# Kernel tuning notes

Hardware: AMD Instinct MI355X
Metric: run time of the kernel (lower is better)

## Reference

```python
import jax, jax.numpy as jnp
import numpy as np

CAPACITY = 0.75      # MoDRouter capacity
ACT_STEPS = 3        # act_max_steps
EPS = 0.01           # ACT halting epsilon
PONDER = 0.01        # act_ponder_cost


def setup_inputs() -> dict:
    key = jax.random.key(0)
    k1, k2, k3 = jax.random.split(key, 3)
    x = jax.random.normal(k1, (4, 8192, 1024), dtype=jnp.float32)
    router_w = jax.random.normal(k2, (1024,), dtype=jnp.float32) * 0.02  # nn.Linear(dim,1,bias=False), std=0.02
    halt_w = jax.random.normal(k3, (1024,), dtype=jnp.float32) * 0.02    # halt linear weight (zeros-init in src; perturbed for nontrivial signal)
    halt_b = -jnp.ones((1,), dtype=jnp.float32)                          # halt bias init -1.0
    return {"x": x, "router_w": router_w, "halt_w": halt_w, "halt_b": halt_b}


def _mod_step(x, router_w):
    """MoDRouter.forward + identity block + MoDRouter.scatter_back."""
    b, s, d = x.shape
    k = max(1, int(s * CAPACITY))
    scores = jnp.einsum('bsd,d->bs', x, router_w)                 # (b, s)
    topk_scores, idx = jax.lax.top_k(scores, k)                   # sorted desc, like torch.topk
    routed = jnp.take_along_axis(x, idx[:, :, None], axis=1)      # (b, k, d) gather
    processed = routed                                            # identity stand-in for Block (undefined in source)
    w = jax.nn.softmax(topk_scores, axis=1)[:, :, None]           # straight-through weights (b, k, 1)
    new_vals = processed * w + (1.0 - w) * routed                 # weighted_processed + (1-w)*original_at_indices
    return x.at[jnp.arange(b)[:, None], idx].set(new_vals)        # scatter back; unrouted tokens = identity


def _act_combine(states, halt_w, halt_b):
    """ACTHaltingUnit.forward: masked accumulation over recurrence steps."""
    b, s, d = states[0].shape
    dt = states[0].dtype
    acc = jnp.zeros((b, s), dt)
    out = jnp.zeros((b, s, d), dt)
    rem = jnp.ones((b, s), dt)
    n_upd = jnp.zeros((b, s), dt)
    for state in states:  # fixed small loop over recurrence steps
        h = jax.nn.sigmoid(jnp.einsum('bsd,d->bs', state, halt_w) + halt_b[0])
        still = (acc < 1.0 - EPS).astype(dt)
        new_acc = acc + h * still
        use_rem = (new_acc > 1.0 - EPS).astype(dt) * still
        use_h = (1.0 - use_rem) * still
        p = use_h * h + use_rem * rem
        out = out + p[:, :, None] * state
        acc = acc + p * still
        rem = rem - p * still
        n_upd = n_upd + still
    ponder_loss = PONDER * jnp.mean(n_upd)
    return out, ponder_loss


def reference(x, router_w, halt_w, halt_b):
    states = []
    cur = x
    for _ in range(ACT_STEPS):
        cur = _mod_step(cur, router_w)
        states.append(cur)
    return _act_combine(states, halt_w, halt_b)
```

## Files before the change

### kernel.cpp

```cpp
#include <hip/hip_runtime.h>
#include <math.h>

#define N_TOKENS 32768
#define DIM      1024
#define WAVES_PER_BLOCK 4

__global__ void modgpt_init(int* __restrict__ n_acc) {
    if (threadIdx.x == 0 && blockIdx.x == 0) n_acc[0] = 0;
}

__global__ __launch_bounds__(256) void modgpt_main(
        const float* __restrict__ x,
        const float* __restrict__ halt_w,
        const float* __restrict__ halt_b,
        float* __restrict__ out,
        int* __restrict__ n_acc) {
    const int wave = threadIdx.x >> 6;
    const int lane = threadIdx.x & 63;
    const int token = blockIdx.x * WAVES_PER_BLOCK + wave;

    const float4* __restrict__ xin = (const float4*)(x + (size_t)token * DIM);
    const float4* __restrict__ w4  = (const float4*)halt_w;

    float4 v0 = xin[lane];
    float4 v1 = xin[lane + 64];
    float4 v2 = xin[lane + 128];
    float4 v3 = xin[lane + 192];
    float4 w0 = w4[lane];
    float4 w1 = w4[lane + 64];
    float4 w2 = w4[lane + 128];
    float4 w3 = w4[lane + 192];

    float dot = v0.x * w0.x + v0.y * w0.y + v0.z * w0.z + v0.w * w0.w
              + v1.x * w1.x + v1.y * w1.y + v1.z * w1.z + v1.w * w1.w
              + v2.x * w2.x + v2.y * w2.y + v2.z * w2.z + v2.w * w2.w
              + v3.x * w3.x + v3.y * w3.y + v3.z * w3.z + v3.w * w3.w;

    #pragma unroll
    for (int off = 32; off >= 1; off >>= 1)
        dot += __shfl_xor(dot, off, 64);

    const float h = 1.0f / (1.0f + expf(-(dot + halt_b[0])));

    float acc = 0.0f, rem = 1.0f, P = 0.0f;
    int n = 0;
    #pragma unroll
    for (int s = 0; s < 3; ++s) {
        if (acc < 0.99f) {
            const float na = acc + h;
            const float p  = (na > 0.99f) ? rem : h;
            P   += p;
            acc += p;
            rem -= p;
            n   += 1;
        }
    }

    float4* __restrict__ o = (float4*)(out + (size_t)token * DIM);
    v0.x *= P; v0.y *= P; v0.z *= P; v0.w *= P;
    v1.x *= P; v1.y *= P; v1.z *= P; v1.w *= P;
    v2.x *= P; v2.y *= P; v2.z *= P; v2.w *= P;
    v3.x *= P; v3.y *= P; v3.z *= P; v3.w *= P;
    o[lane]       = v0;
    o[lane + 64]  = v1;
    o[lane + 128] = v2;
    o[lane + 192] = v3;

    __shared__ int sn[WAVES_PER_BLOCK];
    if (lane == 0) sn[wave] = n;
    __syncthreads();
    if (threadIdx.x == 0)
        atomicAdd(n_acc, sn[0] + sn[1] + sn[2] + sn[3]);
}

__global__ void modgpt_finalize(const int* __restrict__ n_acc,
                                float* __restrict__ ponder_out) {
    if (threadIdx.x == 0 && blockIdx.x == 0)
        ponder_out[0] = 0.01f * ((float)n_acc[0] / (float)N_TOKENS);
}

extern "C" void kernel_launch(void* const* d_in, const int* in_sizes, int n_in,
                              void* d_out, int out_size, void* d_ws, size_t ws_size,
                              hipStream_t stream) {
    const float* x        = (const float*)d_in[0];
    const float* halt_w   = (const float*)d_in[2];
    const float* halt_b   = (const float*)d_in[3];
    float* out            = (float*)d_out;
    int*   n_acc          = (int*)d_ws;

    modgpt_init<<<1, 64, 0, stream>>>(n_acc);
    modgpt_main<<<N_TOKENS / WAVES_PER_BLOCK, 256, 0, stream>>>(
        x, halt_w, halt_b, out, n_acc);
    modgpt_finalize<<<1, 64, 0, stream>>>(n_acc, out + (size_t)N_TOKENS * DIM);
}
```

Before: 272.5 us.

## Process eight tokens per wave with register prefetch and nontemporal stores

Each wave now handles eight consecutive tokens instead of one. It software-pipelines by loading the next token's row while reducing and scaling the current one. The halting weights and bias are loaded once per wave, and the output uses nontemporal stores to avoid polluting cache, with one eighth as many blocks and atomics. The trade-offs are a grid 8x smaller, with fewer waves in flight to hide memory latency, and higher register pressure from the double-buffered rows.

```diff
diff --git a/kernel.cpp b/kernel.cpp
--- a/kernel.cpp
+++ b/kernel.cpp
@@ -4,6 +4,9 @@
 #define N_TOKENS 32768
 #define DIM      1024
 #define WAVES_PER_BLOCK 4
+#define TOK_PER_WAVE 8
+
+typedef float v4f __attribute__((ext_vector_type(4)));
 
 __global__ void modgpt_init(int* __restrict__ n_acc) {
     if (threadIdx.x == 0 && blockIdx.x == 0) n_acc[0] = 0;
@@ -17,57 +20,70 @@
         int* __restrict__ n_acc) {
     const int wave = threadIdx.x >> 6;
     const int lane = threadIdx.x & 63;
-    const int token = blockIdx.x * WAVES_PER_BLOCK + wave;
+    const int token0 = (blockIdx.x * WAVES_PER_BLOCK + wave) * TOK_PER_WAVE;
 
-    const float4* __restrict__ xin = (const float4*)(x + (size_t)token * DIM);
-    const float4* __restrict__ w4  = (const float4*)halt_w;
+    const v4f* __restrict__ xin = (const v4f*)(x + (size_t)token0 * DIM);
+    v4f* __restrict__ oout      = (v4f*)(out + (size_t)token0 * DIM);
+    const v4f* __restrict__ w4  = (const v4f*)halt_w;
 
-    float4 v0 = xin[lane];
-    float4 v1 = xin[lane + 64];
-    float4 v2 = xin[lane + 128];
-    float4 v3 = xin[lane + 192];
-    float4 w0 = w4[lane];
-    float4 w1 = w4[lane + 64];
-    float4 w2 = w4[lane + 128];
-    float4 w3 = w4[lane + 192];
+    const v4f w0 = w4[lane];
+    const v4f w1 = w4[lane + 64];
+    const v4f w2 = w4[lane + 128];
+    const v4f w3 = w4[lane + 192];
+    const float hb = halt_b[0];
 
-    float dot = v0.x * w0.x + v0.y * w0.y + v0.z * w0.z + v0.w * w0.w
-              + v1.x * w1.x + v1.y * w1.y + v1.z * w1.z + v1.w * w1.w
-              + v2.x * w2.x + v2.y * w2.y + v2.z * w2.z + v2.w * w2.w
-              + v3.x * w3.x + v3.y * w3.y + v3.z * w3.z + v3.w * w3.w;
+    int n_sum = 0;
+
+    v4f c0 = xin[lane];
+    v4f c1 = xin[lane + 64];
+    v4f c2 = xin[lane + 128];
+    v4f c3 = xin[lane + 192];
 
     #pragma unroll
-    for (int off = 32; off >= 1; off >>= 1)
-        dot += __shfl_xor(dot, off, 64);
+    for (int t = 0; t < TOK_PER_WAVE; ++t) {
+        v4f p0, p1, p2, p3;
+        if (t + 1 < TOK_PER_WAVE) {
+            const v4f* nx = xin + (size_t)(t + 1) * 256;
+            p0 = nx[lane];
+            p1 = nx[lane + 64];
+            p2 = nx[lane + 128];
+            p3 = nx[lane + 192];
+        }
 
-    const float h = 1.0f / (1.0f + expf(-(dot + halt_b[0])));
+        v4f m = c0 * w0 + c1 * w1 + c2 * w2 + c3 * w3;
+        float dot = m.x + m.y + m.z + m.w;
+        #pragma unroll
+        for (int off = 32; off >= 1; off >>= 1)
+            dot += __shfl_xor(dot, off, 64);
 
-    float acc = 0.0f, rem = 1.0f, P = 0.0f;
-    int n = 0;
-    #pragma unroll
-    for (int s = 0; s < 3; ++s) {
-        if (acc < 0.99f) {
-            const float na = acc + h;
-            const float p  = (na > 0.99f) ? rem : h;
-            P   += p;
-            acc += p;
-            rem -= p;
-            n   += 1;
+        const float h = 1.0f / (1.0f + expf(-(dot + hb)));
+
+        float acc = 0.0f, rem = 1.0f, P = 0.0f;
+        int n = 0;
+        #pragma unroll
+        for (int s = 0; s < 3; ++s) {
+            if (acc < 0.99f) {
+                const float na = acc + h;
+                const float p  = (na > 0.99f) ? rem : h;
+                P   += p;
+                acc += p;
+                rem -= p;
+                n   += 1;
+            }
         }
+        n_sum += n;
+
+        v4f* op = oout + (size_t)t * 256;
+        __builtin_nontemporal_store(c0 * P, op + lane);
+        __builtin_nontemporal_store(c1 * P, op + lane + 64);
+        __builtin_nontemporal_store(c2 * P, op + lane + 128);
+        __builtin_nontemporal_store(c3 * P, op + lane + 192);
+
+        c0 = p0; c1 = p1; c2 = p2; c3 = p3;
     }
 
-    float4* __restrict__ o = (float4*)(out + (size_t)token * DIM);
-    v0.x *= P; v0.y *= P; v0.z *= P; v0.w *= P;
-    v1.x *= P; v1.y *= P; v1.z *= P; v1.w *= P;
-    v2.x *= P; v2.y *= P; v2.z *= P; v2.w *= P;
-    v3.x *= P; v3.y *= P; v3.z *= P; v3.w *= P;
-    o[lane]       = v0;
-    o[lane + 64]  = v1;
-    o[lane + 128] = v2;
-    o[lane + 192] = v3;
-
     __shared__ int sn[WAVES_PER_BLOCK];
-    if (lane == 0) sn[wave] = n;
+    if (lane == 0) sn[wave] = n_sum;
     __syncthreads();
     if (threadIdx.x == 0)
         atomicAdd(n_acc, sn[0] + sn[1] + sn[2] + sn[3]);
@@ -89,7 +105,7 @@
     int*   n_acc          = (int*)d_ws;
 
     modgpt_init<<<1, 64, 0, stream>>>(n_acc);
-    modgpt_main<<<N_TOKENS / WAVES_PER_BLOCK, 256, 0, stream>>>(
+    modgpt_main<<<N_TOKENS / (WAVES_PER_BLOCK * TOK_PER_WAVE), 256, 0, stream>>>(
         x, halt_w, halt_b, out, n_acc);
     modgpt_finalize<<<1, 64, 0, stream>>>(n_acc, out + (size_t)N_TOKENS * DIM);
 }
```

After: 241.7 us. -11.3%, faster.
